# Optimization experiments

Hardware: AMD Instinct MI355X
Metric: run time of the kernel (lower is better)

Reference implementation:

```python
import jax, jax.numpy as jnp
import numpy as np

N_IN = 128
N_H = 64
NEGSAMP_ROUND = 1


def setup_inputs() -> dict:
    key = jax.random.key(0)
    k1, k2, k3, k4 = jax.random.split(key, 4)
    B, S = 8192, 64
    seq1 = jax.random.normal(k1, (B, S, N_IN), dtype=jnp.float32)
    adj = jax.random.uniform(k2, (B, S, S), dtype=jnp.float32)
    # GCN linear (no bias) + separate bias param, xavier-uniform style init
    lim_fc = float(np.sqrt(6.0 / (N_IN + N_H)))
    W_fc = jax.random.uniform(k3, (N_H, N_IN), jnp.float32, -lim_fc, lim_fc)
    b_gcn = jnp.zeros((N_H,), jnp.float32)
    prelu_a = jnp.float32(0.25)  # torch PReLU default single param
    # Bilinear discriminator: weight [1, n_h, n_h], bias [1]
    lim_b = float(np.sqrt(6.0 / (N_H + N_H)))
    W_bil = jax.random.uniform(k4, (1, N_H, N_H), jnp.float32, -lim_b, lim_b)
    b_bil = jnp.zeros((1,), jnp.float32)
    return {"seq1": seq1, "adj": adj, "W_fc": W_fc, "b_gcn": b_gcn,
            "prelu_a": prelu_a, "W_bil": W_bil, "b_bil": b_bil}


def _bilinear(h, c, W_bil, b_bil):
    # nn.Bilinear(n_h, n_h, 1): out[b,o] = sum_ij h[b,i] W[o,i,j] c[b,j] + bias[o]
    return jnp.einsum('bi,oij,bj->bo', h, W_bil, c) + b_bil


def reference(seq1, adj, W_fc, b_gcn, prelu_a, W_bil, b_bil):
    # GCN: linear -> bmm with adjacency -> bias -> PReLU  (fused elementwise)
    seq_fts = jnp.einsum('bsi,hi->bsh', seq1, W_fc)          # [B,S,n_h]
    out = jnp.einsum('bst,bth->bsh', adj, seq_fts) + b_gcn   # [B,S,n_h]
    h_1 = jnp.where(out >= 0, out, prelu_a * out)            # PReLU
    # avg readout over context nodes; last node is the target
    c = jnp.mean(h_1[:, :-1, :], axis=1)                     # [B,n_h]
    h_mv = h_1[:, -1, :]                                     # [B,n_h]
    # Discriminator with batch-shift negative sampling
    scs = [_bilinear(h_mv, c, W_bil, b_bil)]
    c_mi = c
    for _ in range(NEGSAMP_ROUND):
        c_mi = jnp.concatenate([c_mi[-2:-1, :], c_mi[:-1, :]], axis=0)
        scs.append(_bilinear(h_mv, c_mi, W_bil, b_bil))
    logits = jnp.concatenate(scs, axis=0)                    # [(1+r)*B, 1]
    return logits, h_mv, c
```

## Files before the change

### kernel.cpp

```cpp
#include <hip/hip_runtime.h>
#include <hip/hip_bf16.h>

#define BB   8192
#define SS   64
#define NIN  128
#define NH   64
#define NB   8
#define GRID (BB / NB)

typedef __attribute__((ext_vector_type(8))) short  short8;
typedef __attribute__((ext_vector_type(4))) float  f32x4;
typedef __attribute__((ext_vector_type(4))) float  fvec4;


__device__ __forceinline__ short f2bs(float f) {
    union { __hip_bfloat16 h; unsigned short s; } u;
    u.h = __float2bfloat16(f);
    return (short)u.s;
}

__device__ __forceinline__ short8 cvt8(fvec4 x0, fvec4 x1) {
    short8 r;
    #pragma unroll
    for (int i = 0; i < 4; ++i) { r[i] = f2bs(x0[i]); r[i + 4] = f2bs(x1[i]); }
    return r;
}

__device__ __forceinline__ fvec4 ldnt(const fvec4* p) {
    return __builtin_nontemporal_load(p);
}

__global__ __launch_bounds__(256, 4) void fused_gcn(
    const float* __restrict__ seq1, const float* __restrict__ adj,
    const float* __restrict__ W_fc, const float* __restrict__ b_gcn,
    const float* __restrict__ prelu_a, float* __restrict__ out_hmv,
    float* __restrict__ out_c)
{
    __shared__ short8 Wlds[1024];
    __shared__ unsigned short ftsT[2][NH][72];
    __shared__ float c_part[2][4][NH];

    const int tid = threadIdx.x;
    const int w   = tid >> 6;
    const int l   = tid & 63;
    const int m   = l & 15;
    const int g   = l >> 4;
    const int bbase = blockIdx.x * NB;
    const int srow  = 16 * w + m;
    const int s0i   = 16 * w + 4 * g;
    const int fpos  = 32 * (w >> 1) + 8 * g + 4 * (w & 1);

    fvec4 s0, s1, s2, s3, s4, s5, s6, s7;
    fvec4 a0, a1, a2, a3;
    {
        const fvec4* sp = reinterpret_cast<const fvec4*>(seq1 + (size_t)bbase * (SS * NIN) + srow * NIN);
        s0 = ldnt(sp + g);      s1 = ldnt(sp + g + 4);
        s2 = ldnt(sp + g + 8);  s3 = ldnt(sp + g + 12);
        s4 = ldnt(sp + g + 16); s5 = ldnt(sp + g + 20);
        s6 = ldnt(sp + g + 24); s7 = ldnt(sp + g + 28);
        const fvec4* ap = reinterpret_cast<const fvec4*>(adj + (size_t)bbase * (SS * SS) + srow * SS);
        a0 = ldnt(ap + g);      a1 = ldnt(ap + g + 4);
        a2 = ldnt(ap + g + 8);  a3 = ldnt(ap + g + 12);
    }

    #pragma unroll
    for (int kk = 0; kk < 4; ++kk) {
        const fvec4* wp0 = reinterpret_cast<const fvec4*>(W_fc + (16 * w + m) * NIN + 32 * kk + 4 * g);
        Wlds[(w * 4 + kk) * 64 + l] = cvt8(wp0[0], wp0[4]);
    }

    const float pa = *prelu_a;
    float bg[4];
    #pragma unroll
    for (int hj = 0; hj < 4; ++hj) bg[hj] = b_gcn[16 * hj + m];

    asm volatile("s_waitcnt lgkmcnt(0)" ::: "memory");
    __builtin_amdgcn_s_barrier();
    asm volatile("" ::: "memory");

    #pragma unroll 1
    for (int j = 0; j < NB; ++j) {
        const int b = bbase + j;
        const int p = j & 1;

        short8 af[4];
        af[0] = cvt8(s0, s1); af[1] = cvt8(s2, s3);
        af[2] = cvt8(s4, s5); af[3] = cvt8(s6, s7);

        if (j + 1 < NB) {
            const fvec4* sp = reinterpret_cast<const fvec4*>(seq1 + (size_t)(b + 1) * (SS * NIN) + srow * NIN);
            s0 = ldnt(sp + g);      s1 = ldnt(sp + g + 4);
            s2 = ldnt(sp + g + 8);  s3 = ldnt(sp + g + 12);
            s4 = ldnt(sp + g + 16); s5 = ldnt(sp + g + 20);
            s6 = ldnt(sp + g + 24); s7 = ldnt(sp + g + 28);
        }

        f32x4 acc1[4];
        #pragma unroll
        for (int hj = 0; hj < 4; ++hj)
            for (int r = 0; r < 4; ++r) acc1[hj][r] = 0.f;
        #pragma unroll
        for (int hj = 0; hj < 4; ++hj) {
            #pragma unroll
            for (int kk = 0; kk < 4; ++kk) {
                short8 bf = Wlds[(hj * 4 + kk) * 64 + l];
                acc1[hj] = __builtin_amdgcn_mfma_f32_16x16x32_bf16(af[kk], bf, acc1[hj], 0, 0, 0);
            }
        }

        short8 adf0 = cvt8(a0, a1);
        short8 adf1 = cvt8(a2, a3);

        if (j + 1 < NB) {
            const fvec4* ap = reinterpret_cast<const fvec4*>(adj + (size_t)(b + 1) * (SS * SS) + srow * SS);
            a0 = ldnt(ap + g);      a1 = ldnt(ap + g + 4);
            a2 = ldnt(ap + g + 8);  a3 = ldnt(ap + g + 12);
        }

        #pragma unroll
        for (int hj = 0; hj < 4; ++hj) {
            unsigned short q0 = (unsigned short)f2bs(acc1[hj][0]);
            unsigned short q1 = (unsigned short)f2bs(acc1[hj][1]);
            unsigned short q2 = (unsigned short)f2bs(acc1[hj][2]);
            unsigned short q3 = (unsigned short)f2bs(acc1[hj][3]);
            uint2 pk;
            pk.x = (unsigned)q0 | ((unsigned)q1 << 16);
            pk.y = (unsigned)q2 | ((unsigned)q3 << 16);
            *reinterpret_cast<uint2*>(&ftsT[p][16 * hj + m][fpos]) = pk;
        }

        asm volatile("s_waitcnt lgkmcnt(0)" ::: "memory");
        __builtin_amdgcn_s_barrier();
        asm volatile("" ::: "memory");

        f32x4 acc2[4];
        #pragma unroll
        for (int hj = 0; hj < 4; ++hj)
            for (int r = 0; r < 4; ++r) acc2[hj][r] = 0.f;
        #pragma unroll
        for (int hj = 0; hj < 4; ++hj) {
            short8 f0 = *reinterpret_cast<const short8*>(&ftsT[p][16 * hj + m][8 * g]);
            short8 f1 = *reinterpret_cast<const short8*>(&ftsT[p][16 * hj + m][8 * g + 32]);
            acc2[hj] = __builtin_amdgcn_mfma_f32_16x16x32_bf16(adf0, f0, acc2[hj], 0, 0, 0);
            acc2[hj] = __builtin_amdgcn_mfma_f32_16x16x32_bf16(adf1, f1, acc2[hj], 0, 0, 0);
        }

        #pragma unroll
        for (int hj = 0; hj < 4; ++hj) {
            const int h = 16 * hj + m;
            float part = 0.f;
            #pragma unroll
            for (int r = 0; r < 4; ++r) {
                float v = acc2[hj][r] + bg[hj];
                v = (v >= 0.f) ? v : pa * v;
                const int s = s0i + r;
                if (s < SS - 1) part += v;
                else            out_hmv[(size_t)b * NH + h] = v;
            }
            part += __shfl_xor(part, 16);
            part += __shfl_xor(part, 32);
            if (g == 0) c_part[p][w][h] = part;
        }

        if (j > 0 && tid < NH) {
            const int q = p ^ 1;
            float tot = c_part[q][0][tid] + c_part[q][1][tid] + c_part[q][2][tid] + c_part[q][3][tid];
            out_c[(size_t)(b - 1) * NH + tid] = tot * (1.0f / 63.0f);
        }
    }

    asm volatile("s_waitcnt lgkmcnt(0)" ::: "memory");
    __builtin_amdgcn_s_barrier();
    asm volatile("" ::: "memory");
    if (tid < NH) {
        const int q = (NB - 1) & 1;
        float tot = c_part[q][0][tid] + c_part[q][1][tid] + c_part[q][2][tid] + c_part[q][3][tid];
        out_c[(size_t)(bbase + NB - 1) * NH + tid] = tot * (1.0f / 63.0f);
    }
}

__global__ __launch_bounds__(256) void bilinear_k(
    const float* __restrict__ hmv, const float* __restrict__ c,
    const float* __restrict__ wbil, const float* __restrict__ b_bil,
    float* __restrict__ logits)
{
    __shared__ short8 wb[512];

    const int tid = threadIdx.x;
    const int w   = tid >> 6;
    const int l   = tid & 63;
    const int m   = l & 15;
    const int g   = l >> 4;
    const int bgrp = (blockIdx.x * 4 + w) * 16;

    const fvec4* hp = reinterpret_cast<const fvec4*>(hmv + (size_t)(bgrp + m) * NH);
    fvec4 h0 = hp[g], h1 = hp[g + 4], h2 = hp[g + 8], h3 = hp[g + 12];

    short* wbs = reinterpret_cast<short*>(wb);
    for (int q = tid; q < NH * NH; q += 256) {
        int i = q >> 6, jj = q & 63;
        int kk = i >> 5, rem = i & 31;
        int g2, e;
        if (rem < 16) { g2 = rem >> 2;        e = rem & 3; }
        else          { g2 = (rem - 16) >> 2; e = 4 + ((rem - 16) & 3); }
        int nt = jj >> 4, mm = jj & 15;
        wbs[(((kk * 4 + nt) * 64) + g2 * 16 + mm) * 8 + e] = f2bs(wbil[q]);
    }
    __syncthreads();

    short8 af[2];
    af[0] = cvt8(h0, h1);
    af[1] = cvt8(h2, h3);

    f32x4 acc[4];
    #pragma unroll
    for (int nt = 0; nt < 4; ++nt)
        for (int r = 0; r < 4; ++r) acc[nt][r] = 0.f;
    #pragma unroll
    for (int kk = 0; kk < 2; ++kk) {
        #pragma unroll
        for (int nt = 0; nt < 4; ++nt) {
            short8 bf = wb[(kk * 4 + nt) * 64 + l];
            acc[nt] = __builtin_amdgcn_mfma_f32_16x16x32_bf16(af[kk], bf, acc[nt], 0, 0, 0);
        }
    }

    float t0[4] = {0.f, 0.f, 0.f, 0.f};
    float t1[4] = {0.f, 0.f, 0.f, 0.f};
    #pragma unroll
    for (int nt = 0; nt < 4; ++nt) {
        #pragma unroll
        for (int r = 0; r < 4; ++r) {
            const int bq = bgrp + 4 * g + r;
            const int bp = (bq == 0) ? (BB - 2) : (bq - 1);
            float cj = c[(size_t)bq * NH + 16 * nt + m];
            float cp = c[(size_t)bp * NH + 16 * nt + m];
            t0[r] = fmaf(acc[nt][r], cj, t0[r]);
            t1[r] = fmaf(acc[nt][r], cp, t1[r]);
        }
    }
    #pragma unroll
    for (int r = 0; r < 4; ++r) {
        #pragma unroll
        for (int off = 1; off < 16; off <<= 1) {
            t0[r] += __shfl_xor(t0[r], off);
            t1[r] += __shfl_xor(t1[r], off);
        }
    }
    if (m == 0) {
        const float bbv = b_bil[0];
        #pragma unroll
        for (int r = 0; r < 4; ++r) {
            const int bq = bgrp + 4 * g + r;
            logits[bq]      = t0[r] + bbv;
            logits[BB + bq] = t1[r] + bbv;
        }
    }
}

extern "C" void kernel_launch(void* const* d_in, const int* in_sizes, int n_in,
                              void* d_out, int out_size, void* d_ws, size_t ws_size,
                              hipStream_t stream) {
    const float* seq1    = (const float*)d_in[0];
    const float* adj     = (const float*)d_in[1];
    const float* W_fc    = (const float*)d_in[2];
    const float* b_gcn   = (const float*)d_in[3];
    const float* prelu_a = (const float*)d_in[4];
    const float* W_bil   = (const float*)d_in[5];
    const float* b_bil   = (const float*)d_in[6];

    float* out    = (float*)d_out;
    float* logits = out;
    float* hmv    = out + 2 * BB;
    float* cc     = hmv + (size_t)BB * NH;

    fused_gcn<<<GRID, 256, 0, stream>>>(seq1, adj, W_fc, b_gcn, prelu_a, hmv, cc);
    bilinear_k<<<BB / 64, 256, 0, stream>>>(hmv, cc, W_bil, b_bil, logits);
}
```

Before: 83.60 us.

## Fuse bilinear h·W projection into GCN kernel epilogue, simplify logits kernel

Computes v = h_mv·W_bil with MFMA at the end of the fused GCN kernel, using an LDS copy of h_mv in bf16. The result goes to a workspace buffer. A lightweight second kernel then forms the two dot products with c and c shifted by one batch to produce the logits. The aim is to drop the weight re-layout and the MFMA work from the second kernel. In exchange, every GCN block reads W_bil from global memory with scalar loads, which adds latency to the main memory-bound kernel.

```diff
diff --git a/kernel.cpp b/kernel.cpp
--- a/kernel.cpp
+++ b/kernel.cpp
@@ -33,12 +33,14 @@
 __global__ __launch_bounds__(256, 4) void fused_gcn(
     const float* __restrict__ seq1, const float* __restrict__ adj,
     const float* __restrict__ W_fc, const float* __restrict__ b_gcn,
-    const float* __restrict__ prelu_a, float* __restrict__ out_hmv,
-    float* __restrict__ out_c)
+    const float* __restrict__ prelu_a, const float* __restrict__ wbil,
+    float* __restrict__ out_hmv, float* __restrict__ out_c,
+    float* __restrict__ out_v)
 {
     __shared__ short8 Wlds[1024];
     __shared__ unsigned short ftsT[2][NH][72];
     __shared__ float c_part[2][4][NH];
+    __shared__ unsigned short hmv_lds[16][72];
 
     const int tid = threadIdx.x;
     const int w   = tid >> 6;
@@ -155,7 +157,10 @@
                 v = (v >= 0.f) ? v : pa * v;
                 const int s = s0i + r;
                 if (s < SS - 1) part += v;
-                else            out_hmv[(size_t)b * NH + h] = v;
+                else {
+                    out_hmv[(size_t)b * NH + h] = v;
+                    hmv_lds[j][h] = (unsigned short)f2bs(v);
+                }
             }
             part += __shfl_xor(part, 16);
             part += __shfl_xor(part, 32);
@@ -177,84 +182,60 @@
         float tot = c_part[q][0][tid] + c_part[q][1][tid] + c_part[q][2][tid] + c_part[q][3][tid];
         out_c[(size_t)(bbase + NB - 1) * NH + tid] = tot * (1.0f / 63.0f);
     }
-}
-
-__global__ __launch_bounds__(256) void bilinear_k(
-    const float* __restrict__ hmv, const float* __restrict__ c,
-    const float* __restrict__ wbil, const float* __restrict__ b_bil,
-    float* __restrict__ logits)
+
+    {
+        short8 ha[2];
+        #pragma unroll
+        for (int kk = 0; kk < 2; ++kk) {
+            const short8* hrow = reinterpret_cast<const short8*>(&hmv_lds[m][32 * kk + 8 * g]);
+            ha[kk] = hrow[0];
+        }
+        f32x4 acc[4];
+        #pragma unroll
+        for (int nt = 0; nt < 4; ++nt)
+            for (int r = 0; r < 4; ++r) acc[nt][r] = 0.f;
+        #pragma unroll
+        for (int kk = 0; kk < 2; ++kk) {
+            #pragma unroll
+            for (int nt = 0; nt < 4; ++nt) {
+                short8 wf;
+                #pragma unroll
+                for (int e = 0; e < 8; ++e)
+                    wf[e] = f2bs(wbil[(32 * kk + 8 * g + e) * NH + 16 * nt + m]);
+                acc[nt] = __builtin_amdgcn_mfma_f32_16x16x32_bf16(ha[kk], wf, acc[nt], 0, 0, 0);
+            }
+        }
+        if (g < 2) {
+            #pragma unroll
+            for (int nt = 0; nt < 4; ++nt)
+                #pragma unroll
+                for (int r = 0; r < 4; ++r)
+                    out_v[(size_t)(bbase + 4 * g + r) * NH + 16 * nt + m] = acc[nt][r];
+        }
+    }
+}
+
+__global__ __launch_bounds__(256) void logits_k(
+    const float* __restrict__ v, const float* __restrict__ c,
+    const float* __restrict__ b_bil, float* __restrict__ logits)
 {
-    __shared__ short8 wb[512];
-
-    const int tid = threadIdx.x;
-    const int w   = tid >> 6;
-    const int l   = tid & 63;
-    const int m   = l & 15;
-    const int g   = l >> 4;
-    const int bgrp = (blockIdx.x * 4 + w) * 16;
-
-    const fvec4* hp = reinterpret_cast<const fvec4*>(hmv + (size_t)(bgrp + m) * NH);
-    fvec4 h0 = hp[g], h1 = hp[g + 4], h2 = hp[g + 8], h3 = hp[g + 12];
-
-    short* wbs = reinterpret_cast<short*>(wb);
-    for (int q = tid; q < NH * NH; q += 256) {
-        int i = q >> 6, jj = q & 63;
-        int kk = i >> 5, rem = i & 31;
-        int g2, e;
-        if (rem < 16) { g2 = rem >> 2;        e = rem & 3; }
-        else          { g2 = (rem - 16) >> 2; e = 4 + ((rem - 16) & 3); }
-        int nt = jj >> 4, mm = jj & 15;
-        wbs[(((kk * 4 + nt) * 64) + g2 * 16 + mm) * 8 + e] = f2bs(wbil[q]);
-    }
-    __syncthreads();
-
-    short8 af[2];
-    af[0] = cvt8(h0, h1);
-    af[1] = cvt8(h2, h3);
-
-    f32x4 acc[4];
-    #pragma unroll
-    for (int nt = 0; nt < 4; ++nt)
-        for (int r = 0; r < 4; ++r) acc[nt][r] = 0.f;
-    #pragma unroll
-    for (int kk = 0; kk < 2; ++kk) {
-        #pragma unroll
-        for (int nt = 0; nt < 4; ++nt) {
-            short8 bf = wb[(kk * 4 + nt) * 64 + l];
-            acc[nt] = __builtin_amdgcn_mfma_f32_16x16x32_bf16(af[kk], bf, acc[nt], 0, 0, 0);
-        }
-    }
-
-    float t0[4] = {0.f, 0.f, 0.f, 0.f};
-    float t1[4] = {0.f, 0.f, 0.f, 0.f};
-    #pragma unroll
-    for (int nt = 0; nt < 4; ++nt) {
-        #pragma unroll
-        for (int r = 0; r < 4; ++r) {
-            const int bq = bgrp + 4 * g + r;
-            const int bp = (bq == 0) ? (BB - 2) : (bq - 1);
-            float cj = c[(size_t)bq * NH + 16 * nt + m];
-            float cp = c[(size_t)bp * NH + 16 * nt + m];
-            t0[r] = fmaf(acc[nt][r], cj, t0[r]);
-            t1[r] = fmaf(acc[nt][r], cp, t1[r]);
-        }
-    }
-    #pragma unroll
-    for (int r = 0; r < 4; ++r) {
-        #pragma unroll
-        for (int off = 1; off < 16; off <<= 1) {
-            t0[r] += __shfl_xor(t0[r], off);
-            t1[r] += __shfl_xor(t1[r], off);
-        }
-    }
-    if (m == 0) {
+    const int gid = blockIdx.x * 256 + threadIdx.x;
+    const int q   = gid >> 6;
+    const int l   = gid & 63;
+    const int qp  = (q == 0) ? (BB - 2) : (q - 1);
+
+    float vq = v[(size_t)q * NH + l];
+    float t0 = vq * c[(size_t)q  * NH + l];
+    float t1 = vq * c[(size_t)qp * NH + l];
+    #pragma unroll
+    for (int off = 32; off; off >>= 1) {
+        t0 += __shfl_xor(t0, off);
+        t1 += __shfl_xor(t1, off);
+    }
+    if (l == 0) {
         const float bbv = b_bil[0];
-        #pragma unroll
-        for (int r = 0; r < 4; ++r) {
-            const int bq = bgrp + 4 * g + r;
-            logits[bq]      = t0[r] + bbv;
-            logits[BB + bq] = t1[r] + bbv;
-        }
+        logits[q]      = t0 + bbv;
+        logits[BB + q] = t1 + bbv;
     }
 }
 
@@ -274,6 +255,8 @@
     float* hmv    = out + 2 * BB;
     float* cc     = hmv + (size_t)BB * NH;
 
-    fused_gcn<<<GRID, 256, 0, stream>>>(seq1, adj, W_fc, b_gcn, prelu_a, hmv, cc);
-    bilinear_k<<<BB / 64, 256, 0, stream>>>(hmv, cc, W_bil, b_bil, logits);
-}
+    float* v_ws   = (float*)d_ws;
+
+    fused_gcn<<<GRID, 256, 0, stream>>>(seq1, adj, W_fc, b_gcn, prelu_a, W_bil, hmv, cc, v_ws);
+    logits_k<<<BB * 64 / 256, 256, 0, stream>>>(v_ws, cc, b_bil, logits);
+}
```

After: 87.30 us. 1.04x slower.
